# Kernel tuning notes

Hardware: AMD Instinct MI355X
Metric: run time of the kernel (lower is better)

## Reference

```python
import jax, jax.numpy as jnp
import numpy as np

B, N, DIM = 64, 784, 256
N1, N2, HS, WS, M, D = 1, 4, 28, 7, 8, 2  # x_windows, y_windows, H_sp, W_sp, num_heads, d
HW = HS * WS                              # 196 tokens per window
C = DIM // M                              # 32 channels per head


def setup_inputs() -> dict:
    key = jax.random.key(0)
    ks = jax.random.split(key, 5)
    x = jax.random.normal(ks[0], (B, N, DIM), dtype=jnp.float32)
    Wc = jax.random.normal(ks[1], (DIM, M * D), dtype=jnp.float32) * 0.02
    bc = jax.random.normal(ks[2], (M * D,), dtype=jnp.float32) * 0.02
    Wg = jax.random.normal(ks[3], (HW * D, HW * HW), dtype=jnp.float32) * 0.02
    bg = jax.random.normal(ks[4], (HW * HW,), dtype=jnp.float32) * 0.02
    return {"x": x, "Wc": Wc, "bc": bc, "Wg": Wg, "bg": bg}


def reference(x, Wc, bc, Wg, bg):
    b = x.shape[0]
    # compress: B N C -> B N (m d)
    w = x @ Wc + bc
    # rearrange 'b (n1 h n2 w) (m d) -> b (n1 n2 m) (h w d)'
    w = w.reshape(b, N1, HS, N2, WS, M, D)
    w = w.transpose(0, 1, 3, 5, 2, 4, 6).reshape(b, N1 * N2 * M, HW * D)
    # generate per-window mixing weights: B Nw (HW*HW)
    w = w @ Wg + bg
    w = w.reshape(b, N1 * N2 * M, HW, HW)
    # softmax over dim=-2 (the (h1 w1) source axis)
    w = jax.nn.softmax(w, axis=-2)
    # rearrange x: 'b (n1 h1 n2 w1) (m c) -> b (n1 n2 m) c (h1 w1)'
    xv = x.reshape(b, N1, HS, N2, WS, M, C)
    xv = xv.transpose(0, 1, 3, 5, 6, 2, 4).reshape(b, N1 * N2 * M, C, HW)
    # windowed mixing matmul: (b, Nw, C, HW) @ (b, Nw, HW, HW)
    out = jnp.matmul(xv, w)
    # rearrange back: 'b (n1 n2 m) c (h2 w2) -> b (n1 h2 n2 w2) (m c)'
    out = out.reshape(b, N1, N2, M, C, HS, WS)
    out = out.transpose(0, 1, 5, 2, 6, 3, 4).reshape(b, N1 * HS * N2 * WS, M * C)
    return out
```

## Files before the change

kernel.cpp:

```cpp
#include <hip/hip_runtime.h>
#include <hip/hip_bf16.h>
#include <stdint.h>
#include <stddef.h>

#define NB    64
#define NTOK  784
#define DIMC  256
#define NN2   4
#define NM    8
#define NHW   196
#define NWIN  32
#define NROWS 2048
#define NK    392
#define NKP   448
#define NBIG  38416
#define NIP   200
#define STROW 39200
#define STROW2 39232
#define NPT   39296
#define NTT   307
#define PTS   232

typedef __attribute__((ext_vector_type(4))) float f32x4;
typedef __attribute__((ext_vector_type(8))) short bf16x8;

static __device__ __forceinline__ float bf2f(unsigned short u) {
  union { unsigned int i; float f; } v; v.i = ((unsigned int)u) << 16; return v.f;
}
static __device__ __forceinline__ unsigned short f2bf(float f) {
  union { float f; unsigned int i; } v; v.f = f;
  unsigned int r = v.i + 0x7fffu + ((v.i >> 16) & 1u);
  return (unsigned short)(r >> 16);
}

__global__ __launch_bounds__(256) void k_compress(
    const float* __restrict__ x, const float* __restrict__ Wc,
    const float* __restrict__ bc, unsigned short* __restrict__ Abf) {
  __shared__ float wcs[16 * 256];
  __shared__ float bcs[16];
  const int tid = threadIdx.x;
  const int b  = blockIdx.x / NN2;
  const int n2 = blockIdx.x % NN2;
  for (int idx = tid; idx < 4096; idx += 256) {
    int c = idx >> 4, md = idx & 15;
    wcs[md * 256 + c] = Wc[idx];
  }
  if (tid < 16) bcs[tid] = bc[tid];
  __syncthreads();
  if (tid < NHW) {
    const int h = tid / 7, wcol = tid % 7;
    const int t = h * 28 + n2 * 7 + wcol;
    const float* xp = x + ((size_t)b * NTOK + t) * DIMC;
    float acc[16];
    #pragma unroll
    for (int md = 0; md < 16; ++md) acc[md] = bcs[md];
    for (int c = 0; c < 256; c += 4) {
      const f32x4 xv = *(const f32x4*)(xp + c);
      #pragma unroll
      for (int md = 0; md < 16; ++md) {
        const f32x4 wv = *(const f32x4*)(wcs + md * 256 + c);
        acc[md] += xv[0]*wv[0] + xv[1]*wv[1] + xv[2]*wv[2] + xv[3]*wv[3];
      }
    }
    #pragma unroll
    for (int md = 0; md < 16; ++md) {
      const int m = md >> 1, d = md & 1;
      const int r = b * NWIN + n2 * NM + m;
      Abf[(size_t)r * NKP + tid * 2 + d] = f2bf(acc[md]);
    }
  }
  for (int e = tid; e < NM * (NKP - NK); e += 256) {
    const int m = e / (NKP - NK);
    const int k = NK + (e % (NKP - NK));
    const int r = b * NWIN + n2 * NM + m;
    Abf[(size_t)r * NKP + k] = 0;
  }
}

__global__ __launch_bounds__(256) void k_wgt(
    const float* __restrict__ Wg, unsigned short* __restrict__ Wgbt) {
  __shared__ float tile[64][65];
  const int bid = blockIdx.x;
  const int n0 = (bid % 601) * 64;
  const int k0 = (bid / 601) * 64;
  const int tid = threadIdx.x;
  for (int idx = tid; idx < 4096; idx += 256) {
    const int kk = idx >> 6, nn = idx & 63;
    const int k = k0 + kk, n = n0 + nn;
    tile[nn][kk] = (k < NK && n < NBIG) ? Wg[(size_t)k * NBIG + n] : 0.f;
  }
  __syncthreads();
  for (int idx = tid; idx < 4096; idx += 256) {
    const int nn = idx >> 6, kk = idx & 63;
    const int n = n0 + nn;
    if (n < NBIG) {
      const int i = n / NHW, j = n % NHW;
      Wgbt[(size_t)(j * NIP + i) * NKP + (k0 + kk)] = f2bf(tile[nn][kk]);
    }
  }
}

__global__ __launch_bounds__(256) void k_zero(unsigned short* __restrict__ Wgbt) {
  const int j = blockIdx.x >> 2, i = 196 + (blockIdx.x & 3);
  unsigned int* p = (unsigned int*)(Wgbt + (size_t)(j * NIP + i) * NKP);
  if (threadIdx.x < 224) p[threadIdx.x] = 0u;
}

__global__ __launch_bounds__(256) void k_gemm(
    const unsigned short* __restrict__ A,
    const unsigned short* __restrict__ Bt,
    const float* __restrict__ bg,
    unsigned short* __restrict__ S) {
  __shared__ __align__(128) short As[2][128 * 64];
  __shared__ __align__(128) short Bs[2][128 * 64];
  const int tid = threadIdx.x;
  const int w = tid >> 6, lane = tid & 63;
  const int nwg = gridDim.x;
  const int q = nwg >> 3, rr = nwg & 7;
  const int xcd = blockIdx.x & 7, pos = blockIdx.x >> 3;
  const int wg = (xcd < rr ? xcd * (q + 1) : rr * (q + 1) + (xcd - rr) * q) + pos;
  const int mtiles = nwg / NTT;
  const int nt = wg / mtiles, mt = wg % mtiles;
  const int m0 = mt * 128, n0 = nt * 128;
  const int wm = (w >> 1) * 64, wn = (w & 1) * 64;
  const int lrow = lane >> 3;
  const int lcolsw = ((lane & 7) ^ lrow) * 8;

  const unsigned short* Arow = A  + (size_t)(m0 + w * 32 + lrow) * NKP + lcolsw;
  const unsigned short* Brow = Bt + (size_t)(n0 + w * 32 + lrow) * NKP + lcolsw;

  auto stage = [&](int kt, int buf) {
    #pragma unroll
    for (int is = 0; is < 4; ++is) {
      const int gg = w * 4 + is;
      __builtin_amdgcn_global_load_lds(
          (const __attribute__((address_space(1))) void*)(Arow + (size_t)is * 8 * NKP + kt),
          (__attribute__((address_space(3))) void*)((char*)As[buf] + gg * 1024), 16, 0, 0);
      __builtin_amdgcn_global_load_lds(
          (const __attribute__((address_space(1))) void*)(Brow + (size_t)is * 8 * NKP + kt),
          (__attribute__((address_space(3))) void*)((char*)Bs[buf] + gg * 1024), 16, 0, 0);
    }
  };

  f32x4 acc[4][4] = {};
  stage(0, 0);
  __syncthreads();
  const int lq = lane >> 4;
  const int lx = (lane & 7);
  for (int t = 0; t < 7; ++t) {
    const int buf = t & 1;
    if (t < 6) stage((t + 1) * 64, buf ^ 1);
    const short* ab = As[buf];
    const short* bb = Bs[buf];
    #pragma unroll
    for (int kk = 0; kk < 2; ++kk) {
      bf16x8 af[4], bfr[4];
      #pragma unroll
      for (int i = 0; i < 4; ++i) {
        const int row = wm + i * 16 + (lane & 15);
        const int slot = ((kk * 4 + lq) ^ lx) * 8;
        af[i]  = *(const bf16x8*)(ab + row * 64 + slot);
        const int rowb = wn + i * 16 + (lane & 15);
        bfr[i] = *(const bf16x8*)(bb + rowb * 64 + slot);
      }
      #pragma unroll
      for (int mi = 0; mi < 4; ++mi)
        #pragma unroll
        for (int ni = 0; ni < 4; ++ni)
          acc[mi][ni] = __builtin_amdgcn_mfma_f32_16x16x32_bf16(af[mi], bfr[ni], acc[mi][ni], 0, 0, 0);
    }
    __syncthreads();
  }

  #pragma unroll
  for (int ni = 0; ni < 4; ++ni) {
    const int col = n0 + wn + ni * 16 + (lane & 15);
    if (col < STROW) {
      const int i = col % NIP, j = col / NIP;
      const float bgv = (i < NHW) ? bg[i * NHW + j] : 0.f;
      #pragma unroll
      for (int mi = 0; mi < 4; ++mi)
        #pragma unroll
        for (int e = 0; e < 4; ++e) {
          const int row = m0 + wm + mi * 16 + (lane >> 4) * 4 + e;
          S[(size_t)row * STROW2 + col] = f2bf(__expf(acc[mi][ni][e] + bgv));
        }
    } else if (col < STROW2) {
      #pragma unroll
      for (int mi = 0; mi < 4; ++mi)
        #pragma unroll
        for (int e = 0; e < 4; ++e) {
          const int row = m0 + wm + mi * 16 + (lane >> 4) * 4 + e;
          S[(size_t)row * STROW2 + col] = 0;
        }
    }
  }
}

__global__ __launch_bounds__(256) void k_mix(
    const unsigned short* __restrict__ E, const float* __restrict__ x,
    float* __restrict__ out, int row0) {
  __shared__ unsigned short xvT[32 * PTS];
  const int tid = threadIdx.x, w = tid >> 6, lane = tid & 63;
  const int r = row0 + blockIdx.x;
  const int b = r >> 5, win = r & 31, n2 = win >> 3, m = win & 7;

  for (int idx = tid; idx < 1568; idx += 256) {
    const int i = idx >> 3, c4 = (idx & 7) * 4;
    const int t = (i / 7) * 28 + n2 * 7 + (i % 7);
    const f32x4 v = *(const f32x4*)(x + ((size_t)b * NTOK + t) * DIMC + m * 32 + c4);
    xvT[(c4 + 0) * PTS + i] = f2bf(v[0]);
    xvT[(c4 + 1) * PTS + i] = f2bf(v[1]);
    xvT[(c4 + 2) * PTS + i] = f2bf(v[2]);
    xvT[(c4 + 3) * PTS + i] = f2bf(v[3]);
  }
  for (int idx = tid; idx < 32 * (PTS - NHW); idx += 256) {
    const int c = idx / (PTS - NHW), i = NHW + idx % (PTS - NHW);
    xvT[c * PTS + i] = 0;
  }
  __syncthreads();

  bf16x8 bfr[2][7];
  #pragma unroll
  for (int ct = 0; ct < 2; ++ct)
    #pragma unroll
    for (int kk = 0; kk < 7; ++kk)
      bfr[ct][kk] = *(const bf16x8*)&xvT[(ct * 16 + (lane & 15)) * PTS + kk * 32 + (lane >> 4) * 8];
  const bool den = (lane & 15) == 0;
  bf16x8 oneA, oneB;
  #pragma unroll
  for (int e = 0; e < 8; ++e) {
    oneA[e] = den ? (short)0x3F80 : (short)0;
    const int i6 = 192 + (lane >> 4) * 8 + e;
    oneB[e] = (den && i6 < NHW) ? (short)0x3F80 : (short)0;
  }

  const unsigned short* Eb = E + (size_t)blockIdx.x * STROW2;
  for (int jt = w; jt < 13; jt += 4) {
    const int jA = jt * 16 + (lane & 15);
    const unsigned short* rp = Eb + (size_t)(jA < NHW ? jA : NHW - 1) * NIP + (lane >> 4) * 8;
    f32x4 a0 = {0.f,0.f,0.f,0.f}, a1 = {0.f,0.f,0.f,0.f}, ad = {0.f,0.f,0.f,0.f};
    #pragma unroll
    for (int kk = 0; kk < 7; ++kk) {
      const bf16x8 af = *(const bf16x8*)(rp + kk * 32);
      a0 = __builtin_amdgcn_mfma_f32_16x16x32_bf16(af, bfr[0][kk], a0, 0, 0, 0);
      a1 = __builtin_amdgcn_mfma_f32_16x16x32_bf16(af, bfr[1][kk], a1, 0, 0, 0);
      ad = __builtin_amdgcn_mfma_f32_16x16x32_bf16(af, (kk < 6) ? oneA : oneB, ad, 0, 0, 0);
    }
    const int c = lane & 15;
    #pragma unroll
    for (int e = 0; e < 4; ++e) {
      const int j = jt * 16 + (lane >> 4) * 4 + e;
      const float dv = __shfl(ad[e], lane & 48);
      if (j < NHW) {
        const float inv = 1.f / dv;
        const int t2 = (j / 7) * 28 + n2 * 7 + (j % 7);
        float* op = out + ((size_t)b * NTOK + t2) * DIMC + m * 32;
        op[c] = a0[e] * inv;
        op[c + 16] = a1[e] * inv;
      }
    }
  }
}

extern "C" void kernel_launch(void* const* d_in, const int* in_sizes, int n_in,
                              void* d_out, int out_size, void* d_ws, size_t ws_size,
                              hipStream_t stream) {
  const float* x  = (const float*)d_in[0];
  const float* Wc = (const float*)d_in[1];
  const float* bc = (const float*)d_in[2];
  const float* Wg = (const float*)d_in[3];
  const float* bg = (const float*)d_in[4];
  float* out = (float*)d_out;

  char* ws = (char*)d_ws;
  const size_t wgbt_bytes = (size_t)NPT * NKP * 2;
  const size_t a_bytes    = (size_t)NROWS * NKP * 2;
  unsigned short* Wgbt = (unsigned short*)ws;
  unsigned short* Abf  = (unsigned short*)(ws + wgbt_bytes);
  unsigned short* ST   = (unsigned short*)(ws + wgbt_bytes + a_bytes);
  const size_t srow_bytes = (size_t)STROW2 * 2;

  size_t avail = (ws_size > wgbt_bytes + a_bytes) ? (ws_size - wgbt_bytes - a_bytes) : 0;
  int rows_chunk = (int)(avail / srow_bytes);
  rows_chunk = (rows_chunk / 128) * 128;
  if (rows_chunk > NROWS) rows_chunk = NROWS;
  if (rows_chunk < 128)  rows_chunk = 128;

  hipLaunchKernelGGL(k_compress, dim3(NB * NN2), dim3(256), 0, stream, x, Wc, bc, Abf);
  hipLaunchKernelGGL(k_wgt, dim3(601 * 7), dim3(256), 0, stream, Wg, Wgbt);
  hipLaunchKernelGGL(k_zero, dim3(784), dim3(256), 0, stream, Wgbt);
  for (int row0 = 0; row0 < NROWS; row0 += rows_chunk) {
    int rc = NROWS - row0; if (rc > rows_chunk) rc = rows_chunk;
    hipLaunchKernelGGL(k_gemm, dim3((rc / 128) * NTT), dim3(256), 0, stream,
                       Abf + (size_t)row0 * NKP, Wgbt, bg, ST);
    hipLaunchKernelGGL(k_mix, dim3(rc), dim3(256), 0, stream, ST, x, out, row0);
  }
}
```

Before: 256.5 us.

## Fold bias into GEMM K, pre-fragment A, widen N tile to 256

The bias bg is folded into the big GEMM as an extra K column: A gets a ones column and the weight rows get the bias, so the epilogue no longer gathers bg. A is pre-packed into an MFMA fragment layout and read straight from global/L2 into registers instead of being staged through LDS. Each workgroup now covers a 128x256 tile with 8x4 accumulators per wave, which doubles B reuse per tile and halves the N-tile count. The weight transpose is rewritten as one pass per 64 columns with vectorized stores, and k_mix preloads its E fragments. The larger accumulator and register arrays raise register pressure, which may reduce occupancy.

```diff
diff --git a/kernel.cpp b/kernel.cpp
--- a/kernel.cpp
+++ b/kernel.cpp
@@ -13,12 +13,13 @@
 #define NROWS 2048
 #define NK    392
 #define NKP   448
+#define KKF   14
 #define NBIG  38416
 #define NIP   200
 #define STROW 39200
 #define STROW2 39232
-#define NPT   39296
-#define NTT   307
+#define NPT   39424
+#define NTT   154
 #define PTS   232
 
 typedef __attribute__((ext_vector_type(4))) float f32x4;
@@ -73,125 +74,126 @@
     const int m = e / (NKP - NK);
     const int k = NK + (e % (NKP - NK));
     const int r = b * NWIN + n2 * NM + m;
-    Abf[(size_t)r * NKP + k] = 0;
+    Abf[(size_t)r * NKP + k] = (k == NK) ? (unsigned short)0x3F80 : 0;
+  }
+}
+
+__global__ __launch_bounds__(256) void k_afrag(
+    const unsigned short* __restrict__ A, unsigned short* __restrict__ Af) {
+  const int mf = blockIdx.x;
+  for (int idx = threadIdx.x; idx < KKF * 64; idx += 256) {
+    const int kk = idx >> 6, l = idx & 63;
+    const bf16x8 v = *(const bf16x8*)(A + (size_t)(mf * 16 + (l & 15)) * NKP + kk * 32 + (l >> 4) * 8);
+    *(bf16x8*)(Af + ((size_t)(mf * KKF + kk) * 64 + l) * 8) = v;
   }
 }
 
 __global__ __launch_bounds__(256) void k_wgt(
-    const float* __restrict__ Wg, unsigned short* __restrict__ Wgbt) {
-  __shared__ float tile[64][65];
+    const float* __restrict__ Wg, const float* __restrict__ bg,
+    unsigned short* __restrict__ Wgbt) {
+  __shared__ __align__(16) unsigned short tile[64][456];
+  const int n0 = blockIdx.x * 64;
+  const int tid = threadIdx.x;
+  const int ks = tid >> 6, nn = tid & 63;
+  const int n = n0 + nn;
+  for (int k = ks; k < NK; k += 4)
+    tile[nn][k] = f2bf((n < NBIG) ? Wg[(size_t)k * NBIG + n] : 0.f);
+  if (ks == 0) tile[nn][NK] = f2bf((n < NBIG) ? bg[n] : 0.f);
+  for (int k = NK + 1 + ks; k < NKP; k += 4) tile[nn][k] = 0;
+  __syncthreads();
+  for (int idx = tid; idx < 64 * 56; idx += 256) {
+    const int nn2 = idx / 56, g = idx % 56;
+    const int nw = n0 + nn2;
+    if (nw < NBIG) {
+      const int i = nw / NHW, j = nw - i * NHW;
+      const int np = j * NIP + i;
+      *(uint4*)(Wgbt + (size_t)np * NKP + g * 8) = *(const uint4*)&tile[nn2][g * 8];
+    }
+  }
+}
+
+__global__ __launch_bounds__(256) void k_zero(unsigned short* __restrict__ Wgbt) {
   const int bid = blockIdx.x;
-  const int n0 = (bid % 601) * 64;
-  const int k0 = (bid / 601) * 64;
-  const int tid = threadIdx.x;
-  for (int idx = tid; idx < 4096; idx += 256) {
-    const int kk = idx >> 6, nn = idx & 63;
-    const int k = k0 + kk, n = n0 + nn;
-    tile[nn][kk] = (k < NK && n < NBIG) ? Wg[(size_t)k * NBIG + n] : 0.f;
-  }
-  __syncthreads();
-  for (int idx = tid; idx < 4096; idx += 256) {
-    const int nn = idx >> 6, kk = idx & 63;
-    const int n = n0 + nn;
-    if (n < NBIG) {
-      const int i = n / NHW, j = n % NHW;
-      Wgbt[(size_t)(j * NIP + i) * NKP + (k0 + kk)] = f2bf(tile[nn][kk]);
-    }
-  }
-}
-
-__global__ __launch_bounds__(256) void k_zero(unsigned short* __restrict__ Wgbt) {
-  const int j = blockIdx.x >> 2, i = 196 + (blockIdx.x & 3);
-  unsigned int* p = (unsigned int*)(Wgbt + (size_t)(j * NIP + i) * NKP);
+  int np;
+  if (bid < 784) { const int j = bid >> 2, i = 196 + (bid & 3); np = j * NIP + i; }
+  else           { np = STROW + (bid - 784); }
+  unsigned int* p = (unsigned int*)(Wgbt + (size_t)np * NKP);
   if (threadIdx.x < 224) p[threadIdx.x] = 0u;
 }
 
-__global__ __launch_bounds__(256) void k_gemm(
-    const unsigned short* __restrict__ A,
+__global__ __launch_bounds__(256, 2) void k_gemm(
+    const unsigned short* __restrict__ Af,
     const unsigned short* __restrict__ Bt,
-    const float* __restrict__ bg,
-    unsigned short* __restrict__ S) {
-  __shared__ __align__(128) short As[2][128 * 64];
-  __shared__ __align__(128) short Bs[2][128 * 64];
+    unsigned short* __restrict__ E, int row0, int mtiles) {
+  __shared__ __align__(128) short Bs[2][256 * 64];
   const int tid = threadIdx.x;
   const int w = tid >> 6, lane = tid & 63;
   const int nwg = gridDim.x;
   const int q = nwg >> 3, rr = nwg & 7;
   const int xcd = blockIdx.x & 7, pos = blockIdx.x >> 3;
   const int wg = (xcd < rr ? xcd * (q + 1) : rr * (q + 1) + (xcd - rr) * q) + pos;
-  const int mtiles = nwg / NTT;
   const int nt = wg / mtiles, mt = wg % mtiles;
-  const int m0 = mt * 128, n0 = nt * 128;
-  const int wm = (w >> 1) * 64, wn = (w & 1) * 64;
-  const int lrow = lane >> 3;
-  const int lcolsw = ((lane & 7) ^ lrow) * 8;
-
-  const unsigned short* Arow = A  + (size_t)(m0 + w * 32 + lrow) * NKP + lcolsw;
-  const unsigned short* Brow = Bt + (size_t)(n0 + w * 32 + lrow) * NKP + lcolsw;
+  const int n0 = nt * 256;
+  const int lrow = lane >> 3, lgran = lane & 7;
+  const int mf0 = (row0 + mt * 128) >> 4;
+
+  const unsigned short* Ab = Af + (size_t)mf0 * (KKF * 512) + lane * 8;
+  const unsigned short* Bsrc = Bt + (size_t)(n0 + w * 64 + lrow) * NKP + (lgran ^ lrow) * 8;
 
   auto stage = [&](int kt, int buf) {
     #pragma unroll
-    for (int is = 0; is < 4; ++is) {
-      const int gg = w * 4 + is;
+    for (int is = 0; is < 8; ++is) {
+      const int gg = w * 8 + is;
       __builtin_amdgcn_global_load_lds(
-          (const __attribute__((address_space(1))) void*)(Arow + (size_t)is * 8 * NKP + kt),
-          (__attribute__((address_space(3))) void*)((char*)As[buf] + gg * 1024), 16, 0, 0);
-      __builtin_amdgcn_global_load_lds(
-          (const __attribute__((address_space(1))) void*)(Brow + (size_t)is * 8 * NKP + kt),
+          (const __attribute__((address_space(1))) void*)(Bsrc + (size_t)is * 8 * NKP + kt),
           (__attribute__((address_space(3))) void*)((char*)Bs[buf] + gg * 1024), 16, 0, 0);
     }
   };
 
-  f32x4 acc[4][4] = {};
+  f32x4 acc[8][4] = {};
   stage(0, 0);
   __syncthreads();
-  const int lq = lane >> 4;
-  const int lx = (lane & 7);
   for (int t = 0; t < 7; ++t) {
     const int buf = t & 1;
     if (t < 6) stage((t + 1) * 64, buf ^ 1);
-    const short* ab = As[buf];
     const short* bb = Bs[buf];
+    bf16x8 a0[8], a1[8];
+    #pragma unroll
+    for (int mi = 0; mi < 8; ++mi) {
+      a0[mi] = *(const bf16x8*)(Ab + ((size_t)mi * KKF + 2 * t) * 512);
+      a1[mi] = *(const bf16x8*)(Ab + ((size_t)mi * KKF + 2 * t + 1) * 512);
+    }
     #pragma unroll
     for (int kk = 0; kk < 2; ++kk) {
-      bf16x8 af[4], bfr[4];
+      bf16x8 bfr[4];
       #pragma unroll
-      for (int i = 0; i < 4; ++i) {
-        const int row = wm + i * 16 + (lane & 15);
-        const int slot = ((kk * 4 + lq) ^ lx) * 8;
-        af[i]  = *(const bf16x8*)(ab + row * 64 + slot);
-        const int rowb = wn + i * 16 + (lane & 15);
-        bfr[i] = *(const bf16x8*)(bb + rowb * 64 + slot);
+      for (int ni = 0; ni < 4; ++ni) {
+        const int r = w * 64 + ni * 16 + (lane & 15);
+        const int s = (kk * 4 + (lane >> 4)) ^ (lane & 7);
+        bfr[ni] = *(const bf16x8*)(bb + r * 64 + s * 8);
       }
       #pragma unroll
-      for (int mi = 0; mi < 4; ++mi)
+      for (int mi = 0; mi < 8; ++mi)
         #pragma unroll
         for (int ni = 0; ni < 4; ++ni)
-          acc[mi][ni] = __builtin_amdgcn_mfma_f32_16x16x32_bf16(af[mi], bfr[ni], acc[mi][ni], 0, 0, 0);
+          acc[mi][ni] = __builtin_amdgcn_mfma_f32_16x16x32_bf16(
+              kk ? a1[mi] : a0[mi], bfr[ni], acc[mi][ni], 0, 0, 0);
     }
     __syncthreads();
   }
 
+  const int cq = lane >> 4, cr = lane & 15;
+  const int rowbase = mt * 128 + cq * 4;
   #pragma unroll
   for (int ni = 0; ni < 4; ++ni) {
-    const int col = n0 + wn + ni * 16 + (lane & 15);
+    const int col = n0 + w * 64 + ni * 16 + cr;
     if (col < STROW) {
-      const int i = col % NIP, j = col / NIP;
-      const float bgv = (i < NHW) ? bg[i * NHW + j] : 0.f;
       #pragma unroll
-      for (int mi = 0; mi < 4; ++mi)
+      for (int mi = 0; mi < 8; ++mi)
         #pragma unroll
         for (int e = 0; e < 4; ++e) {
-          const int row = m0 + wm + mi * 16 + (lane >> 4) * 4 + e;
-          S[(size_t)row * STROW2 + col] = f2bf(__expf(acc[mi][ni][e] + bgv));
-        }
-    } else if (col < STROW2) {
-      #pragma unroll
-      for (int mi = 0; mi < 4; ++mi)
-        #pragma unroll
-        for (int e = 0; e < 4; ++e) {
-          const int row = m0 + wm + mi * 16 + (lane >> 4) * 4 + e;
-          S[(size_t)row * STROW2 + col] = 0;
+          const int row = rowbase + mi * 16 + e;
+          E[(size_t)row * STROW2 + col] = f2bf(__expf(acc[mi][ni][e]));
         }
     }
   }
@@ -239,13 +241,15 @@
   for (int jt = w; jt < 13; jt += 4) {
     const int jA = jt * 16 + (lane & 15);
     const unsigned short* rp = Eb + (size_t)(jA < NHW ? jA : NHW - 1) * NIP + (lane >> 4) * 8;
+    bf16x8 af[7];
+    #pragma unroll
+    for (int kk = 0; kk < 7; ++kk) af[kk] = *(const bf16x8*)(rp + kk * 32);
     f32x4 a0 = {0.f,0.f,0.f,0.f}, a1 = {0.f,0.f,0.f,0.f}, ad = {0.f,0.f,0.f,0.f};
     #pragma unroll
     for (int kk = 0; kk < 7; ++kk) {
-      const bf16x8 af = *(const bf16x8*)(rp + kk * 32);
-      a0 = __builtin_amdgcn_mfma_f32_16x16x32_bf16(af, bfr[0][kk], a0, 0, 0, 0);
-      a1 = __builtin_amdgcn_mfma_f32_16x16x32_bf16(af, bfr[1][kk], a1, 0, 0, 0);
-      ad = __builtin_amdgcn_mfma_f32_16x16x32_bf16(af, (kk < 6) ? oneA : oneB, ad, 0, 0, 0);
+      a0 = __builtin_amdgcn_mfma_f32_16x16x32_bf16(af[kk], bfr[0][kk], a0, 0, 0, 0);
+      a1 = __builtin_amdgcn_mfma_f32_16x16x32_bf16(af[kk], bfr[1][kk], a1, 0, 0, 0);
+      ad = __builtin_amdgcn_mfma_f32_16x16x32_bf16(af[kk], (kk < 6) ? oneA : oneB, ad, 0, 0, 0);
     }
     const int c = lane & 15;
     #pragma unroll
@@ -276,24 +280,28 @@
   char* ws = (char*)d_ws;
   const size_t wgbt_bytes = (size_t)NPT * NKP * 2;
   const size_t a_bytes    = (size_t)NROWS * NKP * 2;
+  const size_t af_bytes   = (size_t)128 * KKF * 512 * 2;
   unsigned short* Wgbt = (unsigned short*)ws;
   unsigned short* Abf  = (unsigned short*)(ws + wgbt_bytes);
-  unsigned short* ST   = (unsigned short*)(ws + wgbt_bytes + a_bytes);
+  unsigned short* Af   = (unsigned short*)(ws + wgbt_bytes + a_bytes);
+  unsigned short* E    = (unsigned short*)(ws + wgbt_bytes + a_bytes + af_bytes);
+  const size_t fixed = wgbt_bytes + a_bytes + af_bytes;
   const size_t srow_bytes = (size_t)STROW2 * 2;
 
-  size_t avail = (ws_size > wgbt_bytes + a_bytes) ? (ws_size - wgbt_bytes - a_bytes) : 0;
+  size_t avail = (ws_size > fixed) ? (ws_size - fixed) : 0;
   int rows_chunk = (int)(avail / srow_bytes);
   rows_chunk = (rows_chunk / 128) * 128;
   if (rows_chunk > NROWS) rows_chunk = NROWS;
   if (rows_chunk < 128)  rows_chunk = 128;
 
   hipLaunchKernelGGL(k_compress, dim3(NB * NN2), dim3(256), 0, stream, x, Wc, bc, Abf);
-  hipLaunchKernelGGL(k_wgt, dim3(601 * 7), dim3(256), 0, stream, Wg, Wgbt);
-  hipLaunchKernelGGL(k_zero, dim3(784), dim3(256), 0, stream, Wgbt);
+  hipLaunchKernelGGL(k_afrag, dim3(128), dim3(256), 0, stream, Abf, Af);
+  hipLaunchKernelGGL(k_wgt, dim3(601), dim3(256), 0, stream, Wg, bg, Wgbt);
+  hipLaunchKernelGGL(k_zero, dim3(1008), dim3(256), 0, stream, Wgbt);
   for (int row0 = 0; row0 < NROWS; row0 += rows_chunk) {
     int rc = NROWS - row0; if (rc > rows_chunk) rc = rows_chunk;
     hipLaunchKernelGGL(k_gemm, dim3((rc / 128) * NTT), dim3(256), 0, stream,
-                       Abf + (size_t)row0 * NKP, Wgbt, bg, ST);
-    hipLaunchKernelGGL(k_mix, dim3(rc), dim3(256), 0, stream, ST, x, out, row0);
-  }
-}
+                       Af, Wgbt, E, row0, rc / 128);
+    hipLaunchKernelGGL(k_mix, dim3(rc), dim3(256), 0, stream, E, x, out, row0);
+  }
+}
```

After: 341.7 us. +33.2%, slower.
